# Kernel optimization log

Hardware: AMD Instinct MI355X
Metric: run time of the kernel (lower is better)

## Reference

```python
import jax, jax.numpy as jnp
import numpy as np

N_PTS = 131072
K_POSE = 4
J = 24
P_NUM = 64
R_COMP = 32
POSE_DIM = 32
GRID = (512, 512, 128)
MAT_MODE = ((0, 1), (0, 2), (1, 2))


def sample_line(line, xs):
    # line: [k, R, G], xs: [N] in [-1, 1].
    # Equivalent to F.grid_sample on a [k,R,G,1] map with grid x-coord fixed to 0
    # (W==1 so the x dim is degenerate) -> 1D linear interpolation along G.
    G = line.shape[-1]
    pos = (xs + 1.0) * 0.5 * (G - 1)
    i0 = jnp.clip(jnp.floor(pos), 0, G - 1).astype(jnp.int32)
    i1 = jnp.clip(i0 + 1, 0, G - 1)
    w = pos - i0.astype(xs.dtype)
    v0 = jnp.take(line, i0, axis=-1)  # [k,R,N]
    v1 = jnp.take(line, i1, axis=-1)
    return v0 * (1.0 - w) + v1 * w


def blend(w, A):
    # w: [1,N,J], A: [1,J,4,4] -> per-point blended LBS transform [1,N,4,4]
    return jnp.einsum('bnj,bjuv->bnuv', w, A)


def lbs_points(pts, T, inverse):
    Rm = T[..., :3, :3]
    t = T[..., :3, 3]
    if inverse:
        return jnp.einsum('bnij,bnj->bni', jnp.linalg.inv(Rm), pts - t)
    return jnp.einsum('bnij,bnj->bni', Rm, pts) + t


def lbs_dirs(d, T, inverse):
    Rm = T[..., :3, :3]
    if inverse:
        return jnp.einsum('bnij,bnj->bni', jnp.linalg.inv(Rm), d)
    return jnp.einsum('bnij,bnj->bni', Rm, d)


def setup_inputs() -> dict:
    key = jax.random.key(0)
    ks = jax.random.split(key, 12)
    pose_pts = 0.3 * jax.random.normal(ks[0], (1, N_PTS, 3), jnp.float32)
    pose_dirs = jax.random.normal(ks[1], (1, N_PTS, 3), jnp.float32)
    sw = jax.random.uniform(ks[2], (1, N_PTS, J), dtype=jnp.float32)
    skinning_weight = sw / jnp.sum(sw, axis=-1, keepdims=True)
    eye = jnp.eye(4, dtype=jnp.float32)
    A = eye + 0.2 * jax.random.normal(ks[3], (1, J, 4, 4), jnp.float32)
    big_A = eye + 0.2 * jax.random.normal(ks[4], (1, J, 4, 4), jnp.float32)
    tbounds = jnp.array([[-1.5, -1.5, -1.5], [1.5, 1.5, 1.5]], jnp.float32)
    coord_line0 = 0.1 * jax.random.normal(ks[5], (P_NUM, R_COMP, GRID[0], 1), jnp.float32)
    coord_line1 = 0.1 * jax.random.normal(ks[6], (P_NUM, R_COMP, GRID[1], 1), jnp.float32)
    coord_line2 = 0.1 * jax.random.normal(ks[7], (P_NUM, R_COMP, GRID[2], 1), jnp.float32)
    feat_line0 = 0.1 * jax.random.normal(ks[8], (P_NUM, R_COMP, POSE_DIM, 1), jnp.float32)
    feat_line1 = 0.1 * jax.random.normal(ks[9], (P_NUM, R_COMP, POSE_DIM, 1), jnp.float32)
    feat_line2 = 0.1 * jax.random.normal(ks[10], (P_NUM, R_COMP, POSE_DIM, 1), jnp.float32)
    tw = jax.random.uniform(ks[11], (K_POSE,), dtype=jnp.float32) + 0.1
    topk_weight = tw / jnp.sum(tw)  # L1-normalized top-k pose weights
    topk_id = jax.random.randint(jax.random.fold_in(key, 7), (K_POSE,), 0, P_NUM, dtype=jnp.int32)
    return dict(pose_pts=pose_pts, pose_dirs=pose_dirs, skinning_weight=skinning_weight,
                A=A, big_A=big_A, tbounds=tbounds,
                coord_line0=coord_line0, coord_line1=coord_line1, coord_line2=coord_line2,
                feat_line0=feat_line0, feat_line1=feat_line1, feat_line2=feat_line2,
                topk_weight=topk_weight, topk_id=topk_id)


def reference(pose_pts, pose_dirs, skinning_weight, A, big_A, tbounds,
              coord_line0, coord_line1, coord_line2,
              feat_line0, feat_line1, feat_line2,
              topk_weight, topk_id):
    # --- backward_deform: observed pose -> t-pose (inv A) -> big/canonical pose (big_A) ---
    T_A = blend(skinning_weight, A)
    T_big = blend(skinning_weight, big_A)
    tpose = lbs_points(pose_pts, T_A, inverse=True)
    cnl_pts = lbs_points(tpose, T_big, inverse=False)   # [1,N,3]
    tdirs = lbs_dirs(pose_dirs, T_A, inverse=True)
    cnl_dirs = lbs_dirs(tdirs, T_big, inverse=False)    # [1,N,3]
    # --- get_pose_feat: normalize_pts detaches pts, then TensoRF-style line sampling ---
    npts = jax.lax.stop_gradient(cnl_pts)
    npts = (npts - tbounds[0]) / (tbounds[1] - tbounds[0]) * 2.0 - 1.0  # [1,N,3]
    coord_lines = (coord_line0, coord_line1, coord_line2)
    feat_lines = (feat_line0, feat_line1, feat_line2)
    coords, feats = [], []
    for i in range(3):
        line = coord_lines[i][topk_id][..., 0]           # [k,R,G_i]
        coords.append(sample_line(line, npts[0, :, i]))  # [k,R,N]
        feats.append(feat_lines[i][topk_id][..., 0])     # [k,R,C]
    planes = []
    for p, (i0, i1) in enumerate(MAT_MODE):
        t = coords[i0] * coords[i1]                      # [k,R,N] outer-product term
        planes.append(jnp.einsum('krn,krc->knc', t, feats[p]))  # reduce over R
    pose_feats = jnp.concatenate(planes, axis=-1)        # [k,N,3C]
    pose_feat = jnp.sum(topk_weight[:, None, None] * pose_feats, axis=0, keepdims=True)
    return jnp.concatenate([cnl_pts, cnl_dirs, pose_feat], axis=-1)  # [1,N,102]
```

## Files before the change

### kernel.cpp

```cpp
#include <hip/hip_runtime.h>

#define NPTS 131072
#define G0 512
#define G1 512
#define G2 128

#define OFF1 (4*G0*32)
#define OFF2 (4*(G0+G1)*32)
#define LTOT (4*(G0+G1+G2)*32)

#define TRANS_BLOCKS 144
#define FEAT_BLOCKS  48

typedef float v4f __attribute__((ext_vector_type(4)));
typedef _Float16 half8 __attribute__((ext_vector_type(8)));

__device__ unsigned short g_lines16[LTOT + 32];
__device__ unsigned short g_featB[3*4*2*64*8];
__device__ float4 g_pos[NPTS];

__device__ __forceinline__ unsigned short f16bits(float x){
  _Float16 h = (_Float16)x;
  return __builtin_bit_cast(unsigned short, h);
}

#define SKIN_BLOCKS 512
__global__ __launch_bounds__(256) void prep_skin(
    const float* __restrict__ pts, const float* __restrict__ dirs,
    const float* __restrict__ sw,  const float* __restrict__ Am,
    const float* __restrict__ Bm,  const float* __restrict__ tb,
    const float* __restrict__ c0,  const float* __restrict__ c1,
    const float* __restrict__ c2,  const float* __restrict__ f0,
    const float* __restrict__ f1,  const float* __restrict__ f2,
    const float* __restrict__ tw,  const int* __restrict__ topk_id,
    float* __restrict__ out)
{
  const int bid = blockIdx.x;
  const int tid = threadIdx.x;

  if (bid >= SKIN_BLOCKS) {
    int pb = bid - SKIN_BLOCKS;
    if (pb < TRANS_BLOCKS) {
      int e = pb*256 + tid;
      const float* src; int logG, outoff;
      if (e < 16384)      { src = c0; logG = 9; outoff = 0; }
      else if (e < 32768) { e -= 16384; src = c1; logG = 9; outoff = OFF1; }
      else                { e -= 32768; src = c2; logG = 7; outoff = OFF2; }
      const int G = 1 << logG;
      int g  = e & (G-1);
      int t  = e >> logG;
      int r4 = t & 7;
      int kk = t >> 3;
      int id = topk_id[kk];
      const float* s0 = src + (id*32 + r4*4)*G + g;
      float v0 = s0[0];
      float v1 = s0[G];
      float v2 = s0[2*G];
      float v3 = s0[3*G];
      unsigned int lo = ((unsigned int)f16bits(v0)) | (((unsigned int)f16bits(v1)) << 16);
      unsigned int hi = ((unsigned int)f16bits(v2)) | (((unsigned int)f16bits(v3)) << 16);
      uint2 w; w.x = lo; w.y = hi;
      *reinterpret_cast<uint2*>(&g_lines16[outoff + (kk*G + g)*32 + r4*4]) = w;
      return;
    } else {
      int e = (pb - TRANS_BLOCKS)*256 + tid;
      if (e < 3*4*2*64*8) {
        int j    =  e        & 7;
        int lane = (e >> 3)  & 63;
        int tcol = (e >> 9)  & 1;
        int s    = (e >> 10) & 3;
        int p    =  e >> 12;
        int r = ((lane >> 4) << 3) + j;
        int cc = tcol*16 + (lane & 15);
        const float* f = (p == 0) ? f0 : ((p == 1) ? f1 : f2);
        float v = tw[s] * f[(topk_id[s]*32 + r)*32 + cc];
        g_featB[e] = f16bits(v);
      }
      return;
    }
  }

  if (bid == 0 && tid < 32) g_lines16[LTOT + tid] = 0;

  __shared__ float sA[384];
  __shared__ float sB[384];
  for (int i = tid; i < 384; i += 256){ sA[i] = Am[i]; sB[i] = Bm[i]; }
  __syncthreads();

  const int n = bid*256 + tid;
  float swv[24];
  {
    const float4* swp = reinterpret_cast<const float4*>(sw + n*24);
    #pragma unroll
    for (int i = 0; i < 6; i++){
      float4 v = swp[i];
      swv[4*i] = v.x; swv[4*i+1] = v.y; swv[4*i+2] = v.z; swv[4*i+3] = v.w;
    }
  }
  float RA[9] = {0,0,0,0,0,0,0,0,0}, tA[3] = {0,0,0};
  float RB[9] = {0,0,0,0,0,0,0,0,0}, tB[3] = {0,0,0};
  #pragma unroll
  for (int j = 0; j < 24; j++){
    float w = swv[j];
    const float* a = sA + j*16;
    const float* b = sB + j*16;
    RA[0] = fmaf(w, a[0], RA[0]); RA[1] = fmaf(w, a[1], RA[1]); RA[2] = fmaf(w, a[2], RA[2]); tA[0] = fmaf(w, a[3],  tA[0]);
    RA[3] = fmaf(w, a[4], RA[3]); RA[4] = fmaf(w, a[5], RA[4]); RA[5] = fmaf(w, a[6], RA[5]); tA[1] = fmaf(w, a[7],  tA[1]);
    RA[6] = fmaf(w, a[8], RA[6]); RA[7] = fmaf(w, a[9], RA[7]); RA[8] = fmaf(w, a[10],RA[8]); tA[2] = fmaf(w, a[11], tA[2]);
    RB[0] = fmaf(w, b[0], RB[0]); RB[1] = fmaf(w, b[1], RB[1]); RB[2] = fmaf(w, b[2], RB[2]); tB[0] = fmaf(w, b[3],  tB[0]);
    RB[3] = fmaf(w, b[4], RB[3]); RB[4] = fmaf(w, b[5], RB[4]); RB[5] = fmaf(w, b[6], RB[5]); tB[1] = fmaf(w, b[7],  tB[1]);
    RB[6] = fmaf(w, b[8], RB[6]); RB[7] = fmaf(w, b[9], RB[7]); RB[8] = fmaf(w, b[10],RB[8]); tB[2] = fmaf(w, b[11], tB[2]);
  }
  float c00 = RA[4]*RA[8] - RA[5]*RA[7];
  float c01 = RA[5]*RA[6] - RA[3]*RA[8];
  float c02 = RA[3]*RA[7] - RA[4]*RA[6];
  float det = RA[0]*c00 + RA[1]*c01 + RA[2]*c02;
  float idet = 1.0f/det;
  float i00 = c00*idet;
  float i01 = (RA[2]*RA[7] - RA[1]*RA[8])*idet;
  float i02 = (RA[1]*RA[5] - RA[2]*RA[4])*idet;
  float i10 = c01*idet;
  float i11 = (RA[0]*RA[8] - RA[2]*RA[6])*idet;
  float i12 = (RA[2]*RA[3] - RA[0]*RA[5])*idet;
  float i20 = c02*idet;
  float i21 = (RA[1]*RA[6] - RA[0]*RA[7])*idet;
  float i22 = (RA[0]*RA[4] - RA[1]*RA[3])*idet;

  float px = pts[n*3+0], py = pts[n*3+1], pz = pts[n*3+2];
  float dx = dirs[n*3+0], dy = dirs[n*3+1], dz = dirs[n*3+2];
  float qx = px - tA[0], qy = py - tA[1], qz = pz - tA[2];
  float tpx = i00*qx + i01*qy + i02*qz;
  float tpy = i10*qx + i11*qy + i12*qz;
  float tpz = i20*qx + i21*qy + i22*qz;
  float cx = RB[0]*tpx + RB[1]*tpy + RB[2]*tpz + tB[0];
  float cy = RB[3]*tpx + RB[4]*tpy + RB[5]*tpz + tB[1];
  float cz = RB[6]*tpx + RB[7]*tpy + RB[8]*tpz + tB[2];
  float tdx = i00*dx + i01*dy + i02*dz;
  float tdy = i10*dx + i11*dy + i12*dz;
  float tdz = i20*dx + i21*dy + i22*dz;
  float cdx = RB[0]*tdx + RB[1]*tdy + RB[2]*tdz;
  float cdy = RB[3]*tdx + RB[4]*tdy + RB[5]*tdz;
  float cdz = RB[6]*tdx + RB[7]*tdy + RB[8]*tdz;

  {
    float2* o2 = reinterpret_cast<float2*>(out + (size_t)n*102);
    float2 a; a.x = cx;  a.y = cy;
    float2 b; b.x = cz;  b.y = cdx;
    float2 c; c.x = cdy; c.y = cdz;
    o2[0] = a; o2[1] = b; o2[2] = c;
  }
  {
    float lo0 = tb[0], lo1 = tb[1], lo2 = tb[2];
    float hi0 = tb[3], hi1 = tb[4], hi2 = tb[5];
    float x0 = (cx - lo0)/(hi0 - lo0)*2.0f - 1.0f;
    float x1 = (cy - lo1)/(hi1 - lo1)*2.0f - 1.0f;
    float x2 = (cz - lo2)/(hi2 - lo2)*2.0f - 1.0f;
    float4 p;
    p.x = (x0 + 1.0f)*0.5f*(float)(G0-1);
    p.y = (x1 + 1.0f)*0.5f*(float)(G1-1);
    p.z = (x2 + 1.0f)*0.5f*(float)(G2-1);
    p.w = 0.0f;
    g_pos[n] = p;
  }
}

__global__ __launch_bounds__(256) void einsum_mfma(float* __restrict__ out)
{
  const int tid  = threadIdx.x;
  const int lane = tid & 63;
  const int wv   = tid >> 6;
  const int m    = lane & 15;
  const int q    = lane >> 4;
  const int tileBase = (blockIdx.x*4 + wv)*2;

  const unsigned short* lt0 = g_lines16;
  const unsigned short* lt1 = g_lines16 + OFF1;
  const unsigned short* lt2 = g_lines16 + OFF2;
  const half8* fb = reinterpret_cast<const half8*>(g_featB);

  int a0[2], a1[2], a2[2];
  _Float16 w0[2], w1[2], w2[2];
  #pragma unroll
  for (int i = 0; i < 2; i++){
    float4 pos = g_pos[(tileBase + i)*16 + m];
    float pc0 = fminf(fmaxf(pos.x, 0.0f), (float)(G0-1));
    float pc1 = fminf(fmaxf(pos.y, 0.0f), (float)(G1-1));
    float pc2 = fminf(fmaxf(pos.z, 0.0f), (float)(G2-1));
    float fl0 = floorf(pc0), fl1 = floorf(pc1), fl2 = floorf(pc2);
    a0[i] = (int)fl0; a1[i] = (int)fl1; a2[i] = (int)fl2;
    w0[i] = (_Float16)(pc0 - fl0);
    w1[i] = (_Float16)(pc1 - fl1);
    w2[i] = (_Float16)(pc2 - fl2);
  }

  v4f acc[2][6];
  #pragma unroll
  for (int i = 0; i < 2; i++)
    #pragma unroll
    for (int p = 0; p < 6; p++) acc[i][p] = (v4f){0,0,0,0};

  #pragma unroll
  for (int s = 0; s < 4; s++){
    half8 B00 = fb[(0*8 + s*2 + 0)*64 + lane];
    half8 B01 = fb[(0*8 + s*2 + 1)*64 + lane];
    half8 B10 = fb[(1*8 + s*2 + 0)*64 + lane];
    half8 B11 = fb[(1*8 + s*2 + 1)*64 + lane];
    half8 B20 = fb[(2*8 + s*2 + 0)*64 + lane];
    half8 B21 = fb[(2*8 + s*2 + 1)*64 + lane];

    uint4 r0a[2], r1a[2], r0b[2], r1b[2], r0c[2], r1c[2];
    #pragma unroll
    for (int i = 0; i < 2; i++){
      const unsigned short* p0 = lt0 + (s*G0 + a0[i])*32 + q*8;
      r0a[i] = *(const uint4*)p0;  r1a[i] = *(const uint4*)(p0 + 32);
      const unsigned short* p1 = lt1 + (s*G1 + a1[i])*32 + q*8;
      r0b[i] = *(const uint4*)p1;  r1b[i] = *(const uint4*)(p1 + 32);
      const unsigned short* p2 = lt2 + (s*G2 + a2[i])*32 + q*8;
      r0c[i] = *(const uint4*)p2;  r1c[i] = *(const uint4*)(p2 + 32);
    }

    #pragma unroll
    for (int i = 0; i < 2; i++){
      half8 la0 = __builtin_bit_cast(half8, r0a[i]);
      half8 lb0 = __builtin_bit_cast(half8, r1a[i]);
      half8 c0  = la0 + w0[i]*(lb0 - la0);
      half8 la1 = __builtin_bit_cast(half8, r0b[i]);
      half8 lb1 = __builtin_bit_cast(half8, r1b[i]);
      half8 c1  = la1 + w1[i]*(lb1 - la1);
      half8 la2 = __builtin_bit_cast(half8, r0c[i]);
      half8 lb2 = __builtin_bit_cast(half8, r1c[i]);
      half8 c2  = la2 + w2[i]*(lb2 - la2);

      half8 A0 = c0*c1;
      half8 A1 = c0*c2;
      half8 A2 = c1*c2;

      acc[i][0] = __builtin_amdgcn_mfma_f32_16x16x32_f16(A0, B00, acc[i][0], 0, 0, 0);
      acc[i][1] = __builtin_amdgcn_mfma_f32_16x16x32_f16(A0, B01, acc[i][1], 0, 0, 0);
      acc[i][2] = __builtin_amdgcn_mfma_f32_16x16x32_f16(A1, B10, acc[i][2], 0, 0, 0);
      acc[i][3] = __builtin_amdgcn_mfma_f32_16x16x32_f16(A1, B11, acc[i][3], 0, 0, 0);
      acc[i][4] = __builtin_amdgcn_mfma_f32_16x16x32_f16(A2, B20, acc[i][4], 0, 0, 0);
      acc[i][5] = __builtin_amdgcn_mfma_f32_16x16x32_f16(A2, B21, acc[i][5], 0, 0, 0);
    }
  }

  #pragma unroll
  for (int i = 0; i < 2; i++){
    const int rowBase = (tileBase + i)*16 + q*4;
    #pragma unroll
    for (int v = 0; v < 4; v++){
      float* o = out + (size_t)(rowBase + v)*102 + 6 + m;
      o[0]  = acc[i][0][v];
      o[16] = acc[i][1][v];
      o[32] = acc[i][2][v];
      o[48] = acc[i][3][v];
      o[64] = acc[i][4][v];
      o[80] = acc[i][5][v];
    }
  }
}

extern "C" void kernel_launch(void* const* d_in, const int* in_sizes, int n_in,
                              void* d_out, int out_size, void* d_ws, size_t ws_size,
                              hipStream_t stream) {
  const float* pose_pts  = (const float*)d_in[0];
  const float* pose_dirs = (const float*)d_in[1];
  const float* sw        = (const float*)d_in[2];
  const float* Am        = (const float*)d_in[3];
  const float* Bm        = (const float*)d_in[4];
  const float* tb        = (const float*)d_in[5];
  const float* cl0       = (const float*)d_in[6];
  const float* cl1       = (const float*)d_in[7];
  const float* cl2       = (const float*)d_in[8];
  const float* fl0       = (const float*)d_in[9];
  const float* fl1       = (const float*)d_in[10];
  const float* fl2       = (const float*)d_in[11];
  const float* tw        = (const float*)d_in[12];
  const int*   tkid      = (const int*)d_in[13];
  float* out = (float*)d_out;

  hipLaunchKernelGGL(prep_skin, dim3(SKIN_BLOCKS + TRANS_BLOCKS + FEAT_BLOCKS), dim3(256), 0, stream,
                     pose_pts, pose_dirs, sw, Am, Bm, tb,
                     cl0, cl1, cl2, fl0, fl1, fl2, tw, tkid, out);
  hipLaunchKernelGGL(einsum_mfma, dim3(NPTS/(8*16)), dim3(256), 0, stream, out);
}
```

Before: 136.6 us.

## Fuse per-point skinning into MFMA einsum kernel, pass positions via shuffles

Moves the per-point LBS skinning and normalization into the MFMA einsum kernel. Each wave computes 32 points in lanes 0-31 and broadcasts the sampling positions to the MFMA lanes with shuffles, so the g_pos global buffer and its write/read round trip are gone. The line and feature packing now runs in a separate small kernel. In exchange, half the lanes sit idle during skinning, the A/B matrices are read from global memory instead of shared memory, and blocks shrink to 128 threads.

```diff
diff --git a/kernel.cpp b/kernel.cpp
--- a/kernel.cpp
+++ b/kernel.cpp
@@ -17,181 +17,173 @@
 
 __device__ unsigned short g_lines16[LTOT + 32];
 __device__ unsigned short g_featB[3*4*2*64*8];
-__device__ float4 g_pos[NPTS];
 
 __device__ __forceinline__ unsigned short f16bits(float x){
   _Float16 h = (_Float16)x;
   return __builtin_bit_cast(unsigned short, h);
 }
 
-#define SKIN_BLOCKS 512
-__global__ __launch_bounds__(256) void prep_skin(
+__global__ __launch_bounds__(256) void prep_small(
+    const float* __restrict__ c0,  const float* __restrict__ c1,
+    const float* __restrict__ c2,  const float* __restrict__ f0,
+    const float* __restrict__ f1,  const float* __restrict__ f2,
+    const float* __restrict__ tw,  const int* __restrict__ topk_id)
+{
+  const int bid = blockIdx.x;
+  const int tid = threadIdx.x;
+  if (bid == 0 && tid < 32) g_lines16[LTOT + tid] = 0;
+
+  if (bid < TRANS_BLOCKS) {
+    int e = bid*256 + tid;
+    const float* src; int logG, outoff;
+    if (e < 16384)      { src = c0; logG = 9; outoff = 0; }
+    else if (e < 32768) { e -= 16384; src = c1; logG = 9; outoff = OFF1; }
+    else                { e -= 32768; src = c2; logG = 7; outoff = OFF2; }
+    const int G = 1 << logG;
+    int g  = e & (G-1);
+    int t  = e >> logG;
+    int r4 = t & 7;
+    int kk = t >> 3;
+    int id = topk_id[kk];
+    const float* s0 = src + (id*32 + r4*4)*G + g;
+    float v0 = s0[0];
+    float v1 = s0[G];
+    float v2 = s0[2*G];
+    float v3 = s0[3*G];
+    unsigned int lo = ((unsigned int)f16bits(v0)) | (((unsigned int)f16bits(v1)) << 16);
+    unsigned int hi = ((unsigned int)f16bits(v2)) | (((unsigned int)f16bits(v3)) << 16);
+    uint2 w; w.x = lo; w.y = hi;
+    *reinterpret_cast<uint2*>(&g_lines16[outoff + (kk*G + g)*32 + r4*4]) = w;
+  } else {
+    int e = (bid - TRANS_BLOCKS)*256 + tid;
+    if (e < 3*4*2*64*8) {
+      int j    =  e        & 7;
+      int lane = (e >> 3)  & 63;
+      int tcol = (e >> 9)  & 1;
+      int s    = (e >> 10) & 3;
+      int p    =  e >> 12;
+      int r = ((lane >> 4) << 3) + j;
+      int cc = tcol*16 + (lane & 15);
+      const float* f = (p == 0) ? f0 : ((p == 1) ? f1 : f2);
+      float v = tw[s] * f[(topk_id[s]*32 + r)*32 + cc];
+      g_featB[e] = f16bits(v);
+    }
+  }
+}
+
+__global__ __launch_bounds__(128) void fused_all(
     const float* __restrict__ pts, const float* __restrict__ dirs,
     const float* __restrict__ sw,  const float* __restrict__ Am,
     const float* __restrict__ Bm,  const float* __restrict__ tb,
-    const float* __restrict__ c0,  const float* __restrict__ c1,
-    const float* __restrict__ c2,  const float* __restrict__ f0,
-    const float* __restrict__ f1,  const float* __restrict__ f2,
-    const float* __restrict__ tw,  const int* __restrict__ topk_id,
     float* __restrict__ out)
 {
-  const int bid = blockIdx.x;
-  const int tid = threadIdx.x;
-
-  if (bid >= SKIN_BLOCKS) {
-    int pb = bid - SKIN_BLOCKS;
-    if (pb < TRANS_BLOCKS) {
-      int e = pb*256 + tid;
-      const float* src; int logG, outoff;
-      if (e < 16384)      { src = c0; logG = 9; outoff = 0; }
-      else if (e < 32768) { e -= 16384; src = c1; logG = 9; outoff = OFF1; }
-      else                { e -= 32768; src = c2; logG = 7; outoff = OFF2; }
-      const int G = 1 << logG;
-      int g  = e & (G-1);
-      int t  = e >> logG;
-      int r4 = t & 7;
-      int kk = t >> 3;
-      int id = topk_id[kk];
-      const float* s0 = src + (id*32 + r4*4)*G + g;
-      float v0 = s0[0];
-      float v1 = s0[G];
-      float v2 = s0[2*G];
-      float v3 = s0[3*G];
-      unsigned int lo = ((unsigned int)f16bits(v0)) | (((unsigned int)f16bits(v1)) << 16);
-      unsigned int hi = ((unsigned int)f16bits(v2)) | (((unsigned int)f16bits(v3)) << 16);
-      uint2 w; w.x = lo; w.y = hi;
-      *reinterpret_cast<uint2*>(&g_lines16[outoff + (kk*G + g)*32 + r4*4]) = w;
-      return;
-    } else {
-      int e = (pb - TRANS_BLOCKS)*256 + tid;
-      if (e < 3*4*2*64*8) {
-        int j    =  e        & 7;
-        int lane = (e >> 3)  & 63;
-        int tcol = (e >> 9)  & 1;
-        int s    = (e >> 10) & 3;
-        int p    =  e >> 12;
-        int r = ((lane >> 4) << 3) + j;
-        int cc = tcol*16 + (lane & 15);
-        const float* f = (p == 0) ? f0 : ((p == 1) ? f1 : f2);
-        float v = tw[s] * f[(topk_id[s]*32 + r)*32 + cc];
-        g_featB[e] = f16bits(v);
+  const int tid    = threadIdx.x;
+  const int wv     = tid >> 6;
+  const int lane   = tid & 63;
+  const int waveId = blockIdx.x*2 + wv;
+  const int base   = waveId*32;
+
+  float posx = 0.0f, posy = 0.0f, posz = 0.0f;
+
+  if (lane < 32) {
+    const int n = base + lane;
+    float swv[24];
+    {
+      const float4* swp = reinterpret_cast<const float4*>(sw + n*24);
+      #pragma unroll
+      for (int i = 0; i < 6; i++){
+        float4 v = swp[i];
+        swv[4*i] = v.x; swv[4*i+1] = v.y; swv[4*i+2] = v.z; swv[4*i+3] = v.w;
       }
-      return;
-    }
-  }
-
-  if (bid == 0 && tid < 32) g_lines16[LTOT + tid] = 0;
-
-  __shared__ float sA[384];
-  __shared__ float sB[384];
-  for (int i = tid; i < 384; i += 256){ sA[i] = Am[i]; sB[i] = Bm[i]; }
-  __syncthreads();
-
-  const int n = bid*256 + tid;
-  float swv[24];
-  {
-    const float4* swp = reinterpret_cast<const float4*>(sw + n*24);
-    #pragma unroll
-    for (int i = 0; i < 6; i++){
-      float4 v = swp[i];
-      swv[4*i] = v.x; swv[4*i+1] = v.y; swv[4*i+2] = v.z; swv[4*i+3] = v.w;
-    }
-  }
-  float RA[9] = {0,0,0,0,0,0,0,0,0}, tA[3] = {0,0,0};
-  float RB[9] = {0,0,0,0,0,0,0,0,0}, tB[3] = {0,0,0};
-  #pragma unroll
-  for (int j = 0; j < 24; j++){
-    float w = swv[j];
-    const float* a = sA + j*16;
-    const float* b = sB + j*16;
-    RA[0] = fmaf(w, a[0], RA[0]); RA[1] = fmaf(w, a[1], RA[1]); RA[2] = fmaf(w, a[2], RA[2]); tA[0] = fmaf(w, a[3],  tA[0]);
-    RA[3] = fmaf(w, a[4], RA[3]); RA[4] = fmaf(w, a[5], RA[4]); RA[5] = fmaf(w, a[6], RA[5]); tA[1] = fmaf(w, a[7],  tA[1]);
-    RA[6] = fmaf(w, a[8], RA[6]); RA[7] = fmaf(w, a[9], RA[7]); RA[8] = fmaf(w, a[10],RA[8]); tA[2] = fmaf(w, a[11], tA[2]);
-    RB[0] = fmaf(w, b[0], RB[0]); RB[1] = fmaf(w, b[1], RB[1]); RB[2] = fmaf(w, b[2], RB[2]); tB[0] = fmaf(w, b[3],  tB[0]);
-    RB[3] = fmaf(w, b[4], RB[3]); RB[4] = fmaf(w, b[5], RB[4]); RB[5] = fmaf(w, b[6], RB[5]); tB[1] = fmaf(w, b[7],  tB[1]);
-    RB[6] = fmaf(w, b[8], RB[6]); RB[7] = fmaf(w, b[9], RB[7]); RB[8] = fmaf(w, b[10],RB[8]); tB[2] = fmaf(w, b[11], tB[2]);
-  }
-  float c00 = RA[4]*RA[8] - RA[5]*RA[7];
-  float c01 = RA[5]*RA[6] - RA[3]*RA[8];
-  float c02 = RA[3]*RA[7] - RA[4]*RA[6];
-  float det = RA[0]*c00 + RA[1]*c01 + RA[2]*c02;
-  float idet = 1.0f/det;
-  float i00 = c00*idet;
-  float i01 = (RA[2]*RA[7] - RA[1]*RA[8])*idet;
-  float i02 = (RA[1]*RA[5] - RA[2]*RA[4])*idet;
-  float i10 = c01*idet;
-  float i11 = (RA[0]*RA[8] - RA[2]*RA[6])*idet;
-  float i12 = (RA[2]*RA[3] - RA[0]*RA[5])*idet;
-  float i20 = c02*idet;
-  float i21 = (RA[1]*RA[6] - RA[0]*RA[7])*idet;
-  float i22 = (RA[0]*RA[4] - RA[1]*RA[3])*idet;
-
-  float px = pts[n*3+0], py = pts[n*3+1], pz = pts[n*3+2];
-  float dx = dirs[n*3+0], dy = dirs[n*3+1], dz = dirs[n*3+2];
-  float qx = px - tA[0], qy = py - tA[1], qz = pz - tA[2];
-  float tpx = i00*qx + i01*qy + i02*qz;
-  float tpy = i10*qx + i11*qy + i12*qz;
-  float tpz = i20*qx + i21*qy + i22*qz;
-  float cx = RB[0]*tpx + RB[1]*tpy + RB[2]*tpz + tB[0];
-  float cy = RB[3]*tpx + RB[4]*tpy + RB[5]*tpz + tB[1];
-  float cz = RB[6]*tpx + RB[7]*tpy + RB[8]*tpz + tB[2];
-  float tdx = i00*dx + i01*dy + i02*dz;
-  float tdy = i10*dx + i11*dy + i12*dz;
-  float tdz = i20*dx + i21*dy + i22*dz;
-  float cdx = RB[0]*tdx + RB[1]*tdy + RB[2]*tdz;
-  float cdy = RB[3]*tdx + RB[4]*tdy + RB[5]*tdz;
-  float cdz = RB[6]*tdx + RB[7]*tdy + RB[8]*tdz;
-
-  {
-    float2* o2 = reinterpret_cast<float2*>(out + (size_t)n*102);
-    float2 a; a.x = cx;  a.y = cy;
-    float2 b; b.x = cz;  b.y = cdx;
-    float2 c; c.x = cdy; c.y = cdz;
-    o2[0] = a; o2[1] = b; o2[2] = c;
-  }
-  {
-    float lo0 = tb[0], lo1 = tb[1], lo2 = tb[2];
-    float hi0 = tb[3], hi1 = tb[4], hi2 = tb[5];
-    float x0 = (cx - lo0)/(hi0 - lo0)*2.0f - 1.0f;
-    float x1 = (cy - lo1)/(hi1 - lo1)*2.0f - 1.0f;
-    float x2 = (cz - lo2)/(hi2 - lo2)*2.0f - 1.0f;
-    float4 p;
-    p.x = (x0 + 1.0f)*0.5f*(float)(G0-1);
-    p.y = (x1 + 1.0f)*0.5f*(float)(G1-1);
-    p.z = (x2 + 1.0f)*0.5f*(float)(G2-1);
-    p.w = 0.0f;
-    g_pos[n] = p;
-  }
-}
-
-__global__ __launch_bounds__(256) void einsum_mfma(float* __restrict__ out)
-{
-  const int tid  = threadIdx.x;
-  const int lane = tid & 63;
-  const int wv   = tid >> 6;
-  const int m    = lane & 15;
-  const int q    = lane >> 4;
-  const int tileBase = (blockIdx.x*4 + wv)*2;
-
-  const unsigned short* lt0 = g_lines16;
-  const unsigned short* lt1 = g_lines16 + OFF1;
-  const unsigned short* lt2 = g_lines16 + OFF2;
-  const half8* fb = reinterpret_cast<const half8*>(g_featB);
+    }
+    float RA[9] = {0,0,0,0,0,0,0,0,0}, tA[3] = {0,0,0};
+    float RB[9] = {0,0,0,0,0,0,0,0,0}, tB[3] = {0,0,0};
+    #pragma unroll
+    for (int j = 0; j < 24; j++){
+      float w = swv[j];
+      const float* a = Am + j*16;
+      const float* b = Bm + j*16;
+      RA[0] = fmaf(w, a[0], RA[0]); RA[1] = fmaf(w, a[1], RA[1]); RA[2] = fmaf(w, a[2], RA[2]); tA[0] = fmaf(w, a[3],  tA[0]);
+      RA[3] = fmaf(w, a[4], RA[3]); RA[4] = fmaf(w, a[5], RA[4]); RA[5] = fmaf(w, a[6], RA[5]); tA[1] = fmaf(w, a[7],  tA[1]);
+      RA[6] = fmaf(w, a[8], RA[6]); RA[7] = fmaf(w, a[9], RA[7]); RA[8] = fmaf(w, a[10],RA[8]); tA[2] = fmaf(w, a[11], tA[2]);
+      RB[0] = fmaf(w, b[0], RB[0]); RB[1] = fmaf(w, b[1], RB[1]); RB[2] = fmaf(w, b[2], RB[2]); tB[0] = fmaf(w, b[3],  tB[0]);
+      RB[3] = fmaf(w, b[4], RB[3]); RB[4] = fmaf(w, b[5], RB[4]); RB[5] = fmaf(w, b[6], RB[5]); tB[1] = fmaf(w, b[7],  tB[1]);
+      RB[6] = fmaf(w, b[8], RB[6]); RB[7] = fmaf(w, b[9], RB[7]); RB[8] = fmaf(w, b[10],RB[8]); tB[2] = fmaf(w, b[11], tB[2]);
+    }
+    float c00 = RA[4]*RA[8] - RA[5]*RA[7];
+    float c01 = RA[5]*RA[6] - RA[3]*RA[8];
+    float c02 = RA[3]*RA[7] - RA[4]*RA[6];
+    float det = RA[0]*c00 + RA[1]*c01 + RA[2]*c02;
+    float idet = 1.0f/det;
+    float i00 = c00*idet;
+    float i01 = (RA[2]*RA[7] - RA[1]*RA[8])*idet;
+    float i02 = (RA[1]*RA[5] - RA[2]*RA[4])*idet;
+    float i10 = c01*idet;
+    float i11 = (RA[0]*RA[8] - RA[2]*RA[6])*idet;
+    float i12 = (RA[2]*RA[3] - RA[0]*RA[5])*idet;
+    float i20 = c02*idet;
+    float i21 = (RA[1]*RA[6] - RA[0]*RA[7])*idet;
+    float i22 = (RA[0]*RA[4] - RA[1]*RA[3])*idet;
+
+    float px = pts[n*3+0], py = pts[n*3+1], pz = pts[n*3+2];
+    float dx = dirs[n*3+0], dy = dirs[n*3+1], dz = dirs[n*3+2];
+    float qx = px - tA[0], qy = py - tA[1], qz = pz - tA[2];
+    float tpx = i00*qx + i01*qy + i02*qz;
+    float tpy = i10*qx + i11*qy + i12*qz;
+    float tpz = i20*qx + i21*qy + i22*qz;
+    float cx = RB[0]*tpx + RB[1]*tpy + RB[2]*tpz + tB[0];
+    float cy = RB[3]*tpx + RB[4]*tpy + RB[5]*tpz + tB[1];
+    float cz = RB[6]*tpx + RB[7]*tpy + RB[8]*tpz + tB[2];
+    float tdx = i00*dx + i01*dy + i02*dz;
+    float tdy = i10*dx + i11*dy + i12*dz;
+    float tdz = i20*dx + i21*dy + i22*dz;
+    float cdx = RB[0]*tdx + RB[1]*tdy + RB[2]*tdz;
+    float cdy = RB[3]*tdx + RB[4]*tdy + RB[5]*tdz;
+    float cdz = RB[6]*tdx + RB[7]*tdy + RB[8]*tdz;
+
+    {
+      float2* o2 = reinterpret_cast<float2*>(out + (size_t)n*102);
+      float2 a; a.x = cx;  a.y = cy;
+      float2 b; b.x = cz;  b.y = cdx;
+      float2 c; c.x = cdy; c.y = cdz;
+      o2[0] = a; o2[1] = b; o2[2] = c;
+    }
+    {
+      float lo0 = tb[0], lo1 = tb[1], lo2 = tb[2];
+      float hi0 = tb[3], hi1 = tb[4], hi2 = tb[5];
+      float x0 = (cx - lo0)/(hi0 - lo0)*2.0f - 1.0f;
+      float x1 = (cy - lo1)/(hi1 - lo1)*2.0f - 1.0f;
+      float x2 = (cz - lo2)/(hi2 - lo2)*2.0f - 1.0f;
+      posx = (x0 + 1.0f)*0.5f*(float)(G0-1);
+      posy = (x1 + 1.0f)*0.5f*(float)(G1-1);
+      posz = (x2 + 1.0f)*0.5f*(float)(G2-1);
+    }
+  }
+
+  const int m = lane & 15;
+  const int q = lane >> 4;
 
   int a0[2], a1[2], a2[2];
   _Float16 w0[2], w1[2], w2[2];
   #pragma unroll
   for (int i = 0; i < 2; i++){
-    float4 pos = g_pos[(tileBase + i)*16 + m];
-    float pc0 = fminf(fmaxf(pos.x, 0.0f), (float)(G0-1));
-    float pc1 = fminf(fmaxf(pos.y, 0.0f), (float)(G1-1));
-    float pc2 = fminf(fmaxf(pos.z, 0.0f), (float)(G2-1));
+    float px = __shfl(posx, i*16 + m);
+    float py = __shfl(posy, i*16 + m);
+    float pz = __shfl(posz, i*16 + m);
+    float pc0 = fminf(fmaxf(px, 0.0f), (float)(G0-1));
+    float pc1 = fminf(fmaxf(py, 0.0f), (float)(G1-1));
+    float pc2 = fminf(fmaxf(pz, 0.0f), (float)(G2-1));
     float fl0 = floorf(pc0), fl1 = floorf(pc1), fl2 = floorf(pc2);
     a0[i] = (int)fl0; a1[i] = (int)fl1; a2[i] = (int)fl2;
     w0[i] = (_Float16)(pc0 - fl0);
     w1[i] = (_Float16)(pc1 - fl1);
     w2[i] = (_Float16)(pc2 - fl2);
   }
+
+  const unsigned short* lt0 = g_lines16;
+  const unsigned short* lt1 = g_lines16 + OFF1;
+  const unsigned short* lt2 = g_lines16 + OFF2;
+  const half8* fb = reinterpret_cast<const half8*>(g_featB);
 
   v4f acc[2][6];
   #pragma unroll
@@ -246,7 +238,7 @@
 
   #pragma unroll
   for (int i = 0; i < 2; i++){
-    const int rowBase = (tileBase + i)*16 + q*4;
+    const int rowBase = base + i*16 + q*4;
     #pragma unroll
     for (int v = 0; v < 4; v++){
       float* o = out + (size_t)(rowBase + v)*102 + 6 + m;
@@ -279,8 +271,8 @@
   const int*   tkid      = (const int*)d_in[13];
   float* out = (float*)d_out;
 
-  hipLaunchKernelGGL(prep_skin, dim3(SKIN_BLOCKS + TRANS_BLOCKS + FEAT_BLOCKS), dim3(256), 0, stream,
-                     pose_pts, pose_dirs, sw, Am, Bm, tb,
-                     cl0, cl1, cl2, fl0, fl1, fl2, tw, tkid, out);
-  hipLaunchKernelGGL(einsum_mfma, dim3(NPTS/(8*16)), dim3(256), 0, stream, out);
-}
+  hipLaunchKernelGGL(prep_small, dim3(TRANS_BLOCKS + FEAT_BLOCKS), dim3(256), 0, stream,
+                     cl0, cl1, cl2, fl0, fl1, fl2, tw, tkid);
+  hipLaunchKernelGGL(fused_all, dim3(NPTS/64), dim3(128), 0, stream,
+                     pose_pts, pose_dirs, sw, Am, Bm, tb, out);
+}
```

Result: slower. 142.4 us (+4.3%).
